# Kernel tuning notes

Hardware: AMD Instinct MI355X
Metric: run time of the kernel (lower is better)

## Reference

```python
import jax, jax.numpy as jnp
import numpy as np

B_BLK = 64      # sparse_block_size
LOCAL = 4       # sparse_local_num_blocks
GLOB = 2        # sparse_global_num_blocks
STRIDE = 4      # sparse_global_block_stride
NH = 16
NKV = 4
HD = 128
SCALE = HD ** -0.5
NEG = -1e9


def _build_block_index(num_blocks):
    """Static per-query-block key-block index table + validity mask."""
    max_sel = LOCAL + 1 + GLOB
    idx = np.zeros((num_blocks, max_sel), np.int32)
    valid = np.zeros((num_blocks, max_sel), bool)
    for t in range(num_blocks):
        local = list(range(max(0, t - LOCAL), t + 1))
        cand = list(range(0, t + 1, max(1, STRIDE)))
        glob = cand[-GLOB:] if (GLOB > 0 and len(cand) > 0) else []
        sel = sorted(set(local + glob))
        idx[t, :len(sel)] = sel
        valid[t, :len(sel)] = True
    return idx, valid


def _rotate_half(x):
    x1, x2 = jnp.split(x, 2, axis=-1)
    return jnp.concatenate((-x2, x1), axis=-1)


def setup_inputs() -> dict:
    key = jax.random.key(0)
    ks = jax.random.split(key, 7)
    bsz, S, H = 1, 4096, 2048
    return {
        "hidden_states": jax.random.normal(ks[0], (bsz, S, H), jnp.float32) * 0.02,
        "cos": jax.random.uniform(ks[1], (bsz, S, HD), jnp.float32, -1.0, 1.0),
        "sin": jax.random.uniform(ks[2], (bsz, S, HD), jnp.float32, -1.0, 1.0),
        "wq": jax.random.normal(ks[3], (NH * HD, H), jnp.float32) * 0.02,
        "wk": jax.random.normal(ks[4], (NKV * HD, H), jnp.float32) * 0.02,
        "wv": jax.random.normal(ks[5], (NKV * HD, H), jnp.float32) * 0.02,
        "wo": jax.random.normal(ks[6], (H, NH * HD), jnp.float32) * 0.02,
    }


def reference(hidden_states, cos, sin, wq, wk, wv, wo):
    b, S, H = hidden_states.shape
    # QKV projections (nn.Linear: x @ W.T), split heads -> [b, h, S, d]
    q = (hidden_states @ wq.T).reshape(b, S, NH, HD).transpose(0, 2, 1, 3)
    k = (hidden_states @ wk.T).reshape(b, S, NKV, HD).transpose(0, 2, 1, 3)
    v = (hidden_states @ wv.T).reshape(b, S, NKV, HD).transpose(0, 2, 1, 3)
    # RoPE (cos/sin broadcast over heads)
    c = cos[:, None, :, :]
    s = sin[:, None, :, :]
    q = q * c + _rotate_half(q) * s
    k = k * c + _rotate_half(k) * s
    # GQA: repeat KV heads
    n_rep = NH // NKV
    k = jnp.repeat(k, n_rep, axis=1)
    v = jnp.repeat(v, n_rep, axis=1)
    # Block-sparse local+global attention (S divisible by B_BLK -> no padding)
    T = S // B_BLK
    q_blk = q.reshape(b, NH, T, B_BLK, HD)
    k_blk = k.reshape(b, NH, T, B_BLK, HD)
    v_blk = v.reshape(b, NH, T, B_BLK, HD)
    idx, valid = _build_block_index(T)           # [T, Smax] static
    Smax = idx.shape[1]
    k_sel = k_blk[:, :, idx]                     # [b,h,T,Smax,Bk,d]
    v_sel = v_blk[:, :, idx]
    scores = jnp.einsum('bhtqd,bhtspd->bhtqsp', q_blk, k_sel) * SCALE
    # causal intra-block mask on the diagonal block, -inf on padded slots
    intra = jnp.triu(jnp.full((B_BLK, B_BLK), NEG, jnp.float32), 1)
    is_diag = jnp.asarray(idx == np.arange(T)[:, None], jnp.float32)  # [T,Smax]
    mask = is_diag[:, None, :, None] * intra[None, :, None, :]        # [T,Bq,Smax,Bk]
    mask = mask + jnp.where(jnp.asarray(valid)[:, None, :, None], 0.0, NEG)
    scores = scores + mask[None, None]
    scores = scores.reshape(b, NH, T, B_BLK, Smax * B_BLK)
    probs = jax.nn.softmax(scores, axis=-1)
    out = jnp.einsum('bhtqk,bhtkd->bhtqd', probs,
                     v_sel.reshape(b, NH, T, Smax * B_BLK, HD))
    out = out.reshape(b, NH, S, HD).transpose(0, 2, 1, 3).reshape(b, S, NH * HD)
    return out @ wo.T
```

## Files before the change

kernel.cpp:

```cpp
#include <hip/hip_runtime.h>

typedef unsigned short u16;
typedef short bf16x8 __attribute__((ext_vector_type(8)));
typedef float f32x4 __attribute__((ext_vector_type(4)));

#define S_LEN 4096
#define NHEADS 16
#define NKVH 4
#define HDIM 128
#define HID 2048
#define NQKV 3072

__device__ __forceinline__ u16 f2bf(float x) {
  union { float f; unsigned u; } v; v.f = x;
  unsigned r = v.u + 0x7fffu + ((v.u >> 16) & 1u);
  return (u16)(r >> 16);
}
__device__ __forceinline__ float bf2f(u16 x) {
  union { unsigned u; float f; } v; v.u = ((unsigned)x) << 16;
  return v.f;
}
__device__ __forceinline__ void async16(u16* lds, const u16* g) {
  __builtin_amdgcn_global_load_lds((const __attribute__((address_space(1))) void*)g,
                                   (__attribute__((address_space(3))) void*)lds, 16, 0, 0);
}

__global__ __launch_bounds__(256) void cast_all(const float* __restrict__ hs,
                                                const float* __restrict__ wq,
                                                const float* __restrict__ wk,
                                                const float* __restrict__ wv,
                                                const float* __restrict__ wo,
                                                u16* __restrict__ ws) {
  int i = blockIdx.x * 256 + threadIdx.x;
  const float* src; int si;
  if (i < 2097152)      { src = hs; si = i; }
  else if (i < 3145728) { src = wq; si = i - 2097152; }
  else if (i < 3407872) { src = wk; si = i - 3145728; }
  else if (i < 3670016) { src = wv; si = i - 3407872; }
  else                  { src = wo; si = i - 3670016; }
  float4 v = ((const float4*)src)[si];
  ushort4 o;
  o.x = f2bf(v.x); o.y = f2bf(v.y); o.z = f2bf(v.z); o.w = f2bf(v.w);
  ((ushort4*)ws)[i] = o;
}

template<bool OUT_BF16>
__global__ __launch_bounds__(256) void gemm_bt(const u16* __restrict__ A, const u16* __restrict__ B,
                                               void* __restrict__ Cp, int M, int N, int K) {
  __shared__ __align__(16) u16 As[128 * 64];
  __shared__ __align__(16) u16 Bs[128 * 64];
  const int tid = threadIdx.x;
  const int w = tid >> 6, l = tid & 63;
  const int quad = l >> 4, l16 = l & 15;
  const int bm = blockIdx.x, bn = blockIdx.y;
  const int wr = w & 1, wc = w >> 1;

  const size_t abase = (size_t)bm * 128 * K;
  const size_t bbase = (size_t)bn * 128 * K;

  f32x4 acc[4][4];
  for (int i = 0; i < 4; ++i)
    for (int j = 0; j < 4; ++j) acc[i][j] = f32x4{0.f, 0.f, 0.f, 0.f};

  int sm[4], sc[4];
  for (int j = 0; j < 4; ++j) {
    int slot = (w * 4 + j) * 64 + l;
    sm[j] = slot >> 3;
    sc[j] = (slot & 7) ^ (sm[j] & 7);
  }
  int aoff[2][4], boff[2][4];
  for (int ksi = 0; ksi < 2; ++ksi) {
    int cb = ksi * 4 + quad;
    for (int mt = 0; mt < 4; ++mt) {
      int m = wr * 64 + mt * 16 + l16;
      aoff[ksi][mt] = (m * 8 + (cb ^ (m & 7))) * 8;
      int n = wc * 64 + mt * 16 + l16;
      boff[ksi][mt] = (n * 8 + (cb ^ (n & 7))) * 8;
    }
  }

  for (int kt = 0; kt < K; kt += 64) {
    __syncthreads();
    for (int j = 0; j < 4; ++j) {
      async16(&As[(w * 4 + j) * 64 * 8], A + abase + (size_t)sm[j] * K + kt + sc[j] * 8);
      async16(&Bs[(w * 4 + j) * 64 * 8], B + bbase + (size_t)sm[j] * K + kt + sc[j] * 8);
    }
    __syncthreads();
    for (int ksi = 0; ksi < 2; ++ksi) {
      bf16x8 af[4], bv[4];
      for (int mt = 0; mt < 4; ++mt) {
        af[mt] = *(const bf16x8*)&As[aoff[ksi][mt]];
        bv[mt] = *(const bf16x8*)&Bs[boff[ksi][mt]];
      }
      for (int mt = 0; mt < 4; ++mt)
        for (int nt = 0; nt < 4; ++nt)
          acc[mt][nt] = __builtin_amdgcn_mfma_f32_16x16x32_bf16(af[mt], bv[nt], acc[mt][nt], 0, 0, 0);
    }
  }

  const int row_base = bm * 128 + wr * 64;
  const int col_base = bn * 128 + wc * 64;
  for (int mt = 0; mt < 4; ++mt)
    for (int nt = 0; nt < 4; ++nt) {
      int col = col_base + nt * 16 + l16;
      for (int r = 0; r < 4; ++r) {
        int row = row_base + mt * 16 + quad * 4 + r;
        float v = acc[mt][nt][r];
        if (OUT_BF16) ((u16*)Cp)[(size_t)row * N + col] = f2bf(v);
        else          ((float*)Cp)[(size_t)row * N + col] = v;
      }
    }
}

__global__ __launch_bounds__(256) void rope_vtrans(const u16* __restrict__ qkv,
                                                   const float* __restrict__ cosp,
                                                   const float* __restrict__ sinp,
                                                   u16* __restrict__ Q, u16* __restrict__ Kd,
                                                   u16* __restrict__ Vt) {
  __shared__ u16 tile[64][65];
  const int bid = blockIdx.x;
  const int tid = threadIdx.x;
  if (bid < 2560) {
    const float SCALE = 0.08838834764831845f;
    int idx = bid * 256 + tid;
    int d8 = (idx & 7) * 8;
    int hh = (idx >> 3) % 20;
    int s = idx / 160;
    size_t base = (size_t)s * NQKV + hh * 128;

    ushort4 xa = *(const ushort4*)&qkv[base + d8];
    ushort4 xb = *(const ushort4*)&qkv[base + d8 + 4];
    ushort4 ya = *(const ushort4*)&qkv[base + d8 + 64];
    ushort4 yb = *(const ushort4*)&qkv[base + d8 + 68];
    float x[8] = { bf2f(xa.x), bf2f(xa.y), bf2f(xa.z), bf2f(xa.w),
                   bf2f(xb.x), bf2f(xb.y), bf2f(xb.z), bf2f(xb.w) };
    float y[8] = { bf2f(ya.x), bf2f(ya.y), bf2f(ya.z), bf2f(ya.w),
                   bf2f(yb.x), bf2f(yb.y), bf2f(yb.z), bf2f(yb.w) };

    const float* cp = cosp + s * 128 + d8;
    const float* sp = sinp + s * 128 + d8;
    float4 c0 = *(const float4*)(cp);
    float4 c1 = *(const float4*)(cp + 4);
    float4 c2 = *(const float4*)(cp + 64);
    float4 c3 = *(const float4*)(cp + 68);
    float4 s0 = *(const float4*)(sp);
    float4 s1 = *(const float4*)(sp + 4);
    float4 s2 = *(const float4*)(sp + 64);
    float4 s3 = *(const float4*)(sp + 68);
    float cl[8] = { c0.x, c0.y, c0.z, c0.w, c1.x, c1.y, c1.z, c1.w };
    float sl[8] = { s0.x, s0.y, s0.z, s0.w, s1.x, s1.y, s1.z, s1.w };
    float ch[8] = { c2.x, c2.y, c2.z, c2.w, c3.x, c3.y, c3.z, c3.w };
    float sh[8] = { s2.x, s2.y, s2.z, s2.w, s3.x, s3.y, s3.z, s3.w };

    const float g = (hh < NHEADS) ? SCALE : 1.0f;
    u16 o1[8], o2[8];
#pragma unroll
    for (int j = 0; j < 8; ++j) {
      o1[j] = f2bf((x[j] * cl[j] - y[j] * sl[j]) * g);
      o2[j] = f2bf((y[j] * ch[j] + x[j] * sh[j]) * g);
    }
    u16* dst = (hh < NHEADS) ? (Q + ((size_t)hh * S_LEN + s) * HDIM)
                             : (Kd + ((size_t)(hh - NHEADS) * S_LEN + s) * HDIM);
    *(ushort4*)&dst[d8]      = ushort4{o1[0], o1[1], o1[2], o1[3]};
    *(ushort4*)&dst[d8 + 4]  = ushort4{o1[4], o1[5], o1[6], o1[7]};
    *(ushort4*)&dst[d8 + 64] = ushort4{o2[0], o2[1], o2[2], o2[3]};
    *(ushort4*)&dst[d8 + 68] = ushort4{o2[4], o2[5], o2[6], o2[7]};
  } else {
    int vb = bid - 2560;
    int s0 = (vb & 63) * 64;
    int j0 = (vb >> 6) * 64;
    for (int it = 0; it < 16; ++it) {
      int lin = it * 256 + tid;
      int sr = lin >> 6, jc = lin & 63;
      tile[sr][jc] = qkv[(size_t)(s0 + sr) * NQKV + 2560 + j0 + jc];
    }
    __syncthreads();
    for (int it = 0; it < 16; ++it) {
      int lin = it * 256 + tid;
      int dr = lin >> 6, sc = lin & 63;
      Vt[(size_t)(j0 + dr) * S_LEN + s0 + sc] = tile[sc][dr];
    }
  }
}

__global__ __launch_bounds__(256) void attn_kernel(const u16* __restrict__ Q, const u16* __restrict__ K,
                                                   const u16* __restrict__ Vt, u16* __restrict__ Aout) {
  const float NEGF = -30000.0f;
  const int t = blockIdx.x, h = blockIdx.y;
  const int kvh = h >> 2;
  const int tid = threadIdx.x;
  const int w = tid >> 6, l = tid & 63, quad = l >> 4, l16 = l & 15;

  __shared__ __align__(16) u16 Qs[64 * 128];
  __shared__ __align__(16) u16 Ks[64 * 128];
  __shared__ __align__(16) u16 Vs[128 * 64];
  __shared__ __align__(16) u16 Ps[4 * 16 * 72];

  int sel[7]; int nsel = 0;
  {
    int g1 = (t >> 2) << 2, g0 = g1 - 4;
    int lo = t - 4; if (lo < 0) lo = 0;
    if (g0 >= 0 && g0 < lo) sel[nsel++] = g0;
    if (g1 < lo) sel[nsel++] = g1;
    for (int b = lo; b <= t; ++b) sel[nsel++] = b;
  }

  {
    const size_t qbase = ((size_t)h * S_LEN + t * 64) * HDIM;
    for (int j = 0; j < 4; ++j) {
      int slot = (w * 4 + j) * 64 + l;
      int m = slot >> 4;
      int c = (slot & 15) ^ (m & 15);
      async16(&Qs[(w * 4 + j) * 64 * 8], Q + qbase + m * 128 + c * 8);
    }
  }

  float l_run[4];
  for (int r = 0; r < 4; ++r) l_run[r] = 0.f;
  f32x4 oacc[8];
  for (int i = 0; i < 8; ++i) oacc[i] = f32x4{0.f, 0.f, 0.f, 0.f};

  for (int ib = 0; ib < nsel; ++ib) {
    const int kb = sel[ib];
    __syncthreads();
    {
      const size_t kbase = ((size_t)kvh * S_LEN + kb * 64) * HDIM;
      const size_t vbase = (size_t)kvh * HDIM * S_LEN + kb * 64;
      for (int j = 0; j < 4; ++j) {
        int slot = (w * 4 + j) * 64 + l;
        int mk = slot >> 4;
        int ck = (slot & 15) ^ (mk & 15);
        async16(&Ks[(w * 4 + j) * 64 * 8], K + kbase + mk * 128 + ck * 8);
        int dv = slot >> 3;
        int cv = (slot & 7) ^ (dv & 7);
        async16(&Vs[(w * 4 + j) * 64 * 8], Vt + vbase + (size_t)dv * S_LEN + cv * 8);
      }
    }
    __syncthreads();

    f32x4 sacc[4];
    for (int nt = 0; nt < 4; ++nt) sacc[nt] = f32x4{0.f, 0.f, 0.f, 0.f};
    const int mq = w * 16 + l16;
    for (int ks = 0; ks < 128; ks += 32) {
      int cb = (ks >> 3) + quad;
      bf16x8 af = *(const bf16x8*)&Qs[(mq * 16 + (cb ^ (mq & 15))) * 8];
      for (int nt = 0; nt < 4; ++nt) {
        int n = nt * 16 + l16;
        bf16x8 bv = *(const bf16x8*)&Ks[(n * 16 + (cb ^ (n & 15))) * 8];
        sacc[nt] = __builtin_amdgcn_mfma_f32_16x16x32_bf16(af, bv, sacc[nt], 0, 0, 0);
      }
    }

    const bool diag = (kb == t);
    for (int r = 0; r < 4; ++r) {
      int qrow = w * 16 + quad * 4 + r;
      float sum = 0.f;
      for (int nt = 0; nt < 4; ++nt) {
        float v = sacc[nt][r];
        if (diag && (nt * 16 + l16) > qrow) v = NEGF;
        float p = __expf(v);
        sum += p;
        Ps[(w * 16 + quad * 4 + r) * 72 + nt * 16 + l16] = f2bf(p);
      }
      for (int off = 1; off < 16; off <<= 1) sum += __shfl_xor(sum, off);
      l_run[r] += sum;
    }

    for (int ks = 0; ks < 64; ks += 32) {
      bf16x8 pf = *(const bf16x8*)&Ps[(w * 16 + l16) * 72 + ks + quad * 8];
      int cb = (ks >> 3) + quad;
      for (int nt = 0; nt < 8; ++nt) {
        int n = nt * 16 + l16;
        bf16x8 vv = *(const bf16x8*)&Vs[(n * 8 + (cb ^ (n & 7))) * 8];
        oacc[nt] = __builtin_amdgcn_mfma_f32_16x16x32_bf16(pf, vv, oacc[nt], 0, 0, 0);
      }
    }
  }

  float inv[4];
  for (int r = 0; r < 4; ++r) inv[r] = 1.f / l_run[r];
  const int srow = t * 64 + w * 16 + quad * 4;
  for (int nt = 0; nt < 8; ++nt) {
    int col = h * 128 + nt * 16 + l16;
    for (int r = 0; r < 4; ++r)
      Aout[(size_t)(srow + r) * HID + col] = f2bf(oacc[nt][r] * inv[r]);
  }
}

extern "C" void kernel_launch(void* const* d_in, const int* in_sizes, int n_in,
                              void* d_out, int out_size, void* d_ws, size_t ws_size,
                              hipStream_t stream) {
  const float* hs   = (const float*)d_in[0];
  const float* cosp = (const float*)d_in[1];
  const float* sinp = (const float*)d_in[2];
  const float* wq   = (const float*)d_in[3];
  const float* wk   = (const float*)d_in[4];
  const float* wv   = (const float*)d_in[5];
  const float* wo   = (const float*)d_in[6];

  u16* hsb = (u16*)d_ws;
  u16* W   = hsb + (size_t)S_LEN * HID;
  u16* wob = W + (size_t)NQKV * HID;
  u16* qkv = wob + (size_t)HID * HID;
  u16* Qm  = qkv + (size_t)S_LEN * NQKV;
  u16* Km  = Qm + (size_t)NHEADS * S_LEN * HDIM;
  u16* Vt  = Km + (size_t)NKVH * S_LEN * HDIM;
  u16* att = Vt + (size_t)NKVH * HDIM * S_LEN;

  cast_all<<<18432, 256, 0, stream>>>(hs, wq, wk, wv, wo, (u16*)d_ws);

  gemm_bt<true><<<dim3(32, 24), 256, 0, stream>>>(hsb, W, (void*)qkv, 4096, 3072, 2048);
  rope_vtrans<<<3072, 256, 0, stream>>>(qkv, cosp, sinp, Qm, Km, Vt);
  attn_kernel<<<dim3(64, 16), 256, 0, stream>>>(Qm, Km, Vt, att);
  gemm_bt<false><<<dim3(32, 16), 256, 0, stream>>>(att, wob, d_out, 4096, 2048, 2048);
}
```

Baseline: 270.4 us.

## Load Q/K/V MFMA fragments directly from global memory, dropping LDS staging

Q fragments are now held in registers for the whole kernel, and K and V^T fragments are read straight from global memory into MFMA operands for each selected key block. The shared-memory staging of Q/K/V and the two barriers per key block are removed. This saves LDS traffic and synchronisation, but each of the four waves now fetches the same K/V tile separately and relies on cache hits. The V^T reads are strided by the sequence length, so global access is less coalesced.

```diff
diff --git a/kernel.cpp b/kernel.cpp
--- a/kernel.cpp
+++ b/kernel.cpp
@@ -191,9 +191,6 @@
   const int tid = threadIdx.x;
   const int w = tid >> 6, l = tid & 63, quad = l >> 4, l16 = l & 15;
 
-  __shared__ __align__(16) u16 Qs[64 * 128];
-  __shared__ __align__(16) u16 Ks[64 * 128];
-  __shared__ __align__(16) u16 Vs[128 * 64];
   __shared__ __align__(16) u16 Ps[4 * 16 * 72];
 
   int sel[7]; int nsel = 0;
@@ -205,15 +202,11 @@
     for (int b = lo; b <= t; ++b) sel[nsel++] = b;
   }
 
-  {
-    const size_t qbase = ((size_t)h * S_LEN + t * 64) * HDIM;
-    for (int j = 0; j < 4; ++j) {
-      int slot = (w * 4 + j) * 64 + l;
-      int m = slot >> 4;
-      int c = (slot & 15) ^ (m & 15);
-      async16(&Qs[(w * 4 + j) * 64 * 8], Q + qbase + m * 128 + c * 8);
-    }
-  }
+  const int mq = w * 16 + l16;
+  const u16* qptr = Q + ((size_t)h * S_LEN + t * 64 + mq) * HDIM + quad * 8;
+  bf16x8 qf[4];
+#pragma unroll
+  for (int ks = 0; ks < 4; ++ks) qf[ks] = *(const bf16x8*)(qptr + ks * 32);
 
   float l_run[4];
   for (int r = 0; r < 4; ++r) l_run[r] = 0.f;
@@ -222,32 +215,16 @@
 
   for (int ib = 0; ib < nsel; ++ib) {
     const int kb = sel[ib];
-    __syncthreads();
-    {
-      const size_t kbase = ((size_t)kvh * S_LEN + kb * 64) * HDIM;
-      const size_t vbase = (size_t)kvh * HDIM * S_LEN + kb * 64;
-      for (int j = 0; j < 4; ++j) {
-        int slot = (w * 4 + j) * 64 + l;
-        int mk = slot >> 4;
-        int ck = (slot & 15) ^ (mk & 15);
-        async16(&Ks[(w * 4 + j) * 64 * 8], K + kbase + mk * 128 + ck * 8);
-        int dv = slot >> 3;
-        int cv = (slot & 7) ^ (dv & 7);
-        async16(&Vs[(w * 4 + j) * 64 * 8], Vt + vbase + (size_t)dv * S_LEN + cv * 8);
-      }
-    }
-    __syncthreads();
 
     f32x4 sacc[4];
     for (int nt = 0; nt < 4; ++nt) sacc[nt] = f32x4{0.f, 0.f, 0.f, 0.f};
-    const int mq = w * 16 + l16;
-    for (int ks = 0; ks < 128; ks += 32) {
-      int cb = (ks >> 3) + quad;
-      bf16x8 af = *(const bf16x8*)&Qs[(mq * 16 + (cb ^ (mq & 15))) * 8];
+    const u16* kptr = K + ((size_t)kvh * S_LEN + kb * 64) * HDIM + quad * 8;
+#pragma unroll
+    for (int ks = 0; ks < 4; ++ks) {
+#pragma unroll
       for (int nt = 0; nt < 4; ++nt) {
-        int n = nt * 16 + l16;
-        bf16x8 bv = *(const bf16x8*)&Ks[(n * 16 + (cb ^ (n & 15))) * 8];
-        sacc[nt] = __builtin_amdgcn_mfma_f32_16x16x32_bf16(af, bv, sacc[nt], 0, 0, 0);
+        bf16x8 bv = *(const bf16x8*)(kptr + (size_t)(nt * 16 + l16) * HDIM + ks * 32);
+        sacc[nt] = __builtin_amdgcn_mfma_f32_16x16x32_bf16(qf[ks], bv, sacc[nt], 0, 0, 0);
       }
     }
 
@@ -266,12 +243,13 @@
       l_run[r] += sum;
     }
 
+    const u16* vptr = Vt + (size_t)kvh * HDIM * S_LEN + kb * 64 + quad * 8;
+#pragma unroll
     for (int ks = 0; ks < 64; ks += 32) {
       bf16x8 pf = *(const bf16x8*)&Ps[(w * 16 + l16) * 72 + ks + quad * 8];
-      int cb = (ks >> 3) + quad;
+#pragma unroll
       for (int nt = 0; nt < 8; ++nt) {
-        int n = nt * 16 + l16;
-        bf16x8 vv = *(const bf16x8*)&Vs[(n * 8 + (cb ^ (n & 7))) * 8];
+        bf16x8 vv = *(const bf16x8*)(vptr + (size_t)(nt * 16 + l16) * S_LEN + ks);
         oacc[nt] = __builtin_amdgcn_mfma_f32_16x16x32_bf16(pf, vv, oacc[nt], 0, 0, 0);
       }
     }
```

New measurement: 343.3 us. +27.0%, slower.
